# Performance work log

Measured on AMD Instinct MI355X. Metric: run time of the kernel, lower is better.

The kernel has to match this reference:

```python
import jax, jax.numpy as jnp
import numpy as np

N, IN_FEATS, H_FEATS, N_LAYERS, TOP_K, M = 8192, 512, 256, 2, 16, 65536


def setup_inputs() -> dict:
    key = jax.random.key(0)
    ks = jax.random.split(key, 16)
    s = 0.05
    return {
        "src": jax.random.randint(ks[0], (M,), 0, N, dtype=jnp.int32),
        "dst": jax.random.randint(ks[1], (M,), 0, N, dtype=jnp.int32),
        "labels": jax.random.uniform(ks[2], (M,), dtype=jnp.float32),
        "adj": jax.random.uniform(ks[3], (N, N), dtype=jnp.float32),
        "x": jax.random.normal(ks[4], (N, IN_FEATS), dtype=jnp.float32),
        # GNN1 layer weights
        "W1_0": jax.random.normal(ks[5], (IN_FEATS, H_FEATS), dtype=jnp.float32) * s,
        "W1_1": jax.random.normal(ks[6], (H_FEATS, H_FEATS), dtype=jnp.float32) * s,
        # GNN2 layer weights
        "W2_0": jax.random.normal(ks[7], (IN_FEATS, H_FEATS), dtype=jnp.float32) * s,
        "W2_1": jax.random.normal(ks[8], (H_FEATS, H_FEATS), dtype=jnp.float32) * s,
        # similarity-graph attention params
        "W": jax.random.normal(ks[9], (IN_FEATS, H_FEATS), dtype=jnp.float32) * s,
        "a1": jax.random.normal(ks[10], (H_FEATS, 1), dtype=jnp.float32) * s,
        "a2": jax.random.normal(ks[11], (H_FEATS, 1), dtype=jnp.float32) * s,
        # bilinear head: weight [1, in_feats, 2*h_feats], bias [1]
        "bil_w": jax.random.normal(ks[12], (1, IN_FEATS, 2 * H_FEATS), dtype=jnp.float32) * s,
        "bil_b": jnp.zeros((1,), dtype=jnp.float32),
    }


def _adj_norm(a):
    n = a.shape[0]
    a = a + jnp.eye(n, dtype=a.dtype)
    deg = a.sum(axis=0)[:, None]  # column sums, shape [n,1] (matches torch sum(dim=0).unsqueeze(1))
    return a / deg


def _gcn(a, x, weights):
    an = _adj_norm(a)
    z = x
    for Wl in weights:  # dropout=0.0 -> identity
        z = jax.nn.elu(an @ (z @ Wl))
    return z


def _sim_graph(x, W, a1, a2, top_k):
    n = x.shape[0]
    h = x @ W                      # [n, h]
    s1 = h @ a1                    # [n, 1]
    s2 = (h @ a2).reshape(1, n)    # [1, n]
    a = s1 + s2 - jnp.eye(n, dtype=x.dtype) * 1e15
    a = jax.nn.softmax(jax.nn.leaky_relu(a, 0.2), axis=1)
    kth = jax.lax.top_k(a, top_k)[0][:, -1:]  # k-th largest per row
    m = a >= kth
    m = m | m.T
    return m.astype(x.dtype)


def reference(src, dst, labels, adj, x, W1_0, W1_1, W2_0, W2_1, W, a1, a2, bil_w, bil_b):
    h = _gcn(adj, x, [W1_0, W1_1])
    sim_adj = _sim_graph(x, W, a1, a2, TOP_K)
    h_ = _gcn(sim_adj, x, [W2_0, W2_1])
    h_cat = jnp.concatenate([h, h_], axis=1)          # [n, 2h]
    src_h = x[src]                                    # [m, in_feats]
    dst_h = h_cat[dst]                                # [m, 2h]
    logits = jnp.einsum('mi,ij,mj->m', src_h, bil_w[0], dst_h) + bil_b[0]
    # BCEWithLogitsLoss (mean), numerically stable
    loss = jnp.mean(jnp.maximum(logits, 0.0) - logits * labels + jnp.log1p(jnp.exp(-jnp.abs(logits))))
    predict = logits >= 0
    return (loss, logits, predict)
```

## Files before the change

### kernel.cpp

```cpp
#include <hip/hip_runtime.h>
#include <math.h>

#define NN    8192
#define FIN   512
#define HF    256
#define ME    65536

typedef _Float16 f16x8 __attribute__((ext_vector_type(8)));
typedef __fp16 pk16x2 __attribute__((ext_vector_type(2)));
typedef float f32x4  __attribute__((ext_vector_type(4)));

__device__ inline void split_pk(float a0, float a1, unsigned& hi, unsigned& lo) {
    pk16x2 h = __builtin_amdgcn_cvt_pkrtz(a0, a1);
    float r0 = a0 - (float)h[0];
    float r1 = a1 - (float)h[1];
    pk16x2 l = __builtin_amdgcn_cvt_pkrtz(r0, r1);
    hi = __builtin_bit_cast(unsigned, h);
    lo = __builtin_bit_cast(unsigned, l);
}
__device__ inline unsigned pack_f16rn(float a0, float a1) {
    _Float16 h0 = (_Float16)a0, h1 = (_Float16)a1;
    unsigned u0 = (unsigned)__builtin_bit_cast(unsigned short, h0);
    unsigned u1 = (unsigned)__builtin_bit_cast(unsigned short, h1);
    return u0 | (u1 << 16);
}
__device__ inline unsigned short f16rn(float v) {
    return __builtin_bit_cast(unsigned short, (_Float16)v);
}
__device__ inline void split_f16(float v, short& hi, short& lo) {
    _Float16 h = (_Float16)v;
    _Float16 l = (_Float16)(v - (float)h);
    hi = __builtin_bit_cast(short, h);
    lo = __builtin_bit_cast(short, l);
}
__device__ inline float eluf(float v) { return v > 0.f ? v : expm1f(v); }

__device__ inline void gload16(const void* g, void* l) {
    __builtin_amdgcn_global_load_lds(
        (const __attribute__((address_space(1))) unsigned int*)g,
        (__attribute__((address_space(3))) unsigned int*)l, 16, 0, 0);
}

__global__ __launch_bounds__(256) void colsum_cv(const float* __restrict__ adj,
                                                 float* __restrict__ deg,
                                                 unsigned short* __restrict__ adjh) {
    int c = (blockIdx.x * 256 + threadIdx.x) * 4;
    int r0 = blockIdx.y * 64;
    float4 s = make_float4(0.f, 0.f, 0.f, 0.f);
    for (int r = r0; r < r0 + 64; ++r) {
        float4 v = *(const float4*)(adj + (size_t)r * NN + c);
        s.x += v.x; s.y += v.y; s.z += v.z; s.w += v.w;
        if (adjh) {
            ushort4 h;
            h.x = f16rn(v.x); h.y = f16rn(v.y); h.z = f16rn(v.z); h.w = f16rn(v.w);
            *(ushort4*)(adjh + (size_t)r * NN + c) = h;
        }
    }
    if (blockIdx.y == 0) { s.x += 1.f; s.y += 1.f; s.z += 1.f; s.w += 1.f; }
    atomicAdd(&deg[c + 0], s.x);
    atomicAdd(&deg[c + 1], s.y);
    atomicAdd(&deg[c + 2], s.z);
    atomicAdd(&deg[c + 3], s.w);
}

__global__ __launch_bounds__(256) void trans_w_split(const float* __restrict__ src,
                                                     short* __restrict__ dsth,
                                                     short* __restrict__ dstl,
                                                     int K, int lgN) {
    int idx = blockIdx.x * 256 + threadIdx.x;
    int N = 1 << lgN;
    int k = idx >> lgN, n = idx & (N - 1);
    short h, l;
    split_f16(src[idx], h, l);
    dsth[(size_t)n * K + k] = h;
    dstl[(size_t)n * K + k] = l;
}

template <int PASSES, int WBT>
__global__ __launch_bounds__(256, 2) void mfma_gemm(
    const float* __restrict__ A, const short* __restrict__ BtH,
    const short* __restrict__ BtL, float* __restrict__ C,
    short* __restrict__ CtH, short* __restrict__ CtL, int M, int K, int N)
{
    __shared__ __align__(16) char smem[49152];
    char* sAh = smem;
    char* sAl = smem + 8192;
    char* sBh = smem + 16384;
    char* sBl = smem + 32768;
    float* sT = (float*)smem;
    const int tid = threadIdx.x, lane = tid & 63, wid = tid >> 6;
    const int wm = wid >> 1, wn = wid & 1;
    const int m0 = blockIdx.x * 64, n0 = blockIdx.y * 128;
    const int lhi = lane >> 4, llo = lane & 15;

    f32x4 acc[2][4];
    #pragma unroll
    for (int mi = 0; mi < 2; ++mi)
        #pragma unroll
        for (int ni = 0; ni < 4; ++ni) acc[mi][ni] = (f32x4){0.f, 0.f, 0.f, 0.f};

    for (int kt = 0; kt < K; kt += 64) {
        float4 av[4];
        #pragma unroll
        for (int it = 0; it < 4; ++it) {
            int h = tid + 256 * it;
            int r = h >> 4, hs = h & 15, slot = hs >> 1, half = hs & 1;
            int gk = ((slot ^ (r & 7)) * 2 + half) * 4;
            av[it] = *(const float4*)(A + (size_t)(m0 + r) * K + kt + gk);
        }
        __syncthreads();
        #pragma unroll
        for (int it = 0; it < 4; ++it) {
            int u = tid + 256 * it;
            int c = u >> 3, s = u & 7;
            size_t off = (size_t)(n0 + c) * K + kt + (s ^ (c & 7)) * 8;
            gload16(BtH + off, sBh + u * 16);
            gload16(BtL + off, sBl + u * 16);
        }
        #pragma unroll
        for (int it = 0; it < 4; ++it) {
            int h = tid + 256 * it;
            if (PASSES == 3) {
                uint2 wh, wl;
                split_pk(av[it].x, av[it].y, wh.x, wl.x);
                split_pk(av[it].z, av[it].w, wh.y, wl.y);
                *(uint2*)(sAh + h * 8) = wh;
                *(uint2*)(sAl + h * 8) = wl;
            } else {
                uint2 wh;
                wh.x = pack_f16rn(av[it].x, av[it].y);
                wh.y = pack_f16rn(av[it].z, av[it].w);
                *(uint2*)(sAh + h * 8) = wh;
            }
        }
        __syncthreads();
        #pragma unroll
        for (int ks = 0; ks < 2; ++ks) {
            f16x8 afh[2], afl[2], bfh[4], bfl[4];
            #pragma unroll
            for (int mi = 0; mi < 2; ++mi) {
                int R = wm * 32 + mi * 16 + llo;
                int boff = R * 128 + (((ks * 4 + lhi) ^ (R & 7)) << 4);
                afh[mi] = *(const f16x8*)(sAh + boff);
                if (PASSES == 3) afl[mi] = *(const f16x8*)(sAl + boff);
            }
            #pragma unroll
            for (int ni = 0; ni < 4; ++ni) {
                int Cc = wn * 64 + ni * 16 + llo;
                int boff = Cc * 128 + (((ks * 4 + lhi) ^ (Cc & 7)) << 4);
                bfh[ni] = *(const f16x8*)(sBh + boff);
                bfl[ni] = *(const f16x8*)(sBl + boff);
            }
            #pragma unroll
            for (int mi = 0; mi < 2; ++mi)
                #pragma unroll
                for (int ni = 0; ni < 4; ++ni) {
                    acc[mi][ni] = __builtin_amdgcn_mfma_f32_16x16x32_f16(afh[mi], bfh[ni], acc[mi][ni], 0, 0, 0);
                    acc[mi][ni] = __builtin_amdgcn_mfma_f32_16x16x32_f16(afh[mi], bfl[ni], acc[mi][ni], 0, 0, 0);
                    if (PASSES == 3)
                        acc[mi][ni] = __builtin_amdgcn_mfma_f32_16x16x32_f16(afl[mi], bfh[ni], acc[mi][ni], 0, 0, 0);
                }
        }
    }

    if (WBT) {
        __syncthreads();
        #pragma unroll
        for (int mi = 0; mi < 2; ++mi)
            #pragma unroll
            for (int ni = 0; ni < 4; ++ni) {
                int lr = wm * 32 + mi * 16 + lhi * 4;
                int lc = wn * 64 + ni * 16 + llo;
                int R0 = m0 + lr;
                int Cc = n0 + lc;
                #pragma unroll
                for (int r = 0; r < 4; ++r) {
                    C[(size_t)(R0 + r) * N + Cc] = acc[mi][ni][r];
                    sT[(lr + r) * 136 + lc] = acc[mi][ni][r];
                }
            }
        __syncthreads();
        int c = tid >> 1, ih = (tid & 1) * 32;
        unsigned bh[16], bl[16];
        #pragma unroll
        for (int j = 0; j < 32; j += 2)
            split_pk(sT[(ih + j) * 136 + c], sT[(ih + j + 1) * 136 + c],
                     bh[j >> 1], bl[j >> 1]);
        int4* dh = (int4*)(CtH + (size_t)(n0 + c) * M + m0 + ih);
        int4* dl = (int4*)(CtL + (size_t)(n0 + c) * M + m0 + ih);
        #pragma unroll
        for (int q = 0; q < 4; ++q) { dh[q] = ((int4*)bh)[q]; dl[q] = ((int4*)bl)[q]; }
    } else {
        #pragma unroll
        for (int mi = 0; mi < 2; ++mi)
            #pragma unroll
            for (int ni = 0; ni < 4; ++ni) {
                int R0 = m0 + wm * 32 + mi * 16 + lhi * 4;
                int Cc = n0 + wn * 64 + ni * 16 + llo;
                #pragma unroll
                for (int r = 0; r < 4; ++r)
                    C[(size_t)(R0 + r) * N + Cc] = acc[mi][ni][r];
            }
    }
}

__global__ __launch_bounds__(256, 4) void adj_prop_g(const unsigned short* __restrict__ adjh,
                                                     const short* __restrict__ YtH,
                                                     const short* __restrict__ YtL,
                                                     float* part0, float* part1)
{
    __shared__ __align__(16) char smem[24576];
    const int tid = threadIdx.x, lane = tid & 63, wid = tid >> 6;
    const int wm = wid >> 1, wn = wid & 1;
    const int bid = blockIdx.x;
    const int g  = bid & 7;
    const int ky = g >> 2;
    const int gx = g & 3;
    const int s  = bid >> 3;
    const int bm = gx * 32 + (s >> 2), bn = s & 3;
    const int i0 = bm * 64, c0 = bn * 64;
    const int kbase = ky * (NN / 2);
    const int lhi = lane >> 4, llo = lane & 15;

    f32x4 acc[2][2];
    #pragma unroll
    for (int mi = 0; mi < 2; ++mi)
        #pragma unroll
        for (int ni = 0; ni < 2; ++ni) acc[mi][ni] = (f32x4){0.f, 0.f, 0.f, 0.f};

    for (int t = 0; t < 64; ++t) {
        const int KT = kbase + t * 64;
        __syncthreads();
        #pragma unroll
        for (int it = 0; it < 2; ++it) {
            int u = tid + 256 * it;
            int r = u >> 3, sq = u & 7;
            gload16(adjh + (size_t)(i0 + r) * NN + KT + ((sq ^ (r & 7)) * 8),
                    smem + u * 16);
        }
        #pragma unroll
        for (int it = 0; it < 2; ++it) {
            int u = tid + 256 * it;
            int c = u >> 3, sq = u & 7;
            size_t off = (size_t)(c0 + c) * NN + KT + (sq ^ (c & 7)) * 8;
            gload16(YtH + off, smem + 8192 + u * 16);
            gload16(YtL + off, smem + 16384 + u * 16);
        }
        __syncthreads();
        {
            const char* ah = smem;
            const char* bh = smem + 8192;
            const char* bl = smem + 16384;
            #pragma unroll
            for (int ks = 0; ks < 2; ++ks) {
                f16x8 af[2], bfh[2], bfl[2];
                #pragma unroll
                for (int mi = 0; mi < 2; ++mi) {
                    int R = wm * 32 + mi * 16 + llo;
                    int boff = R * 128 + (((ks * 4 + lhi) ^ (R & 7)) << 4);
                    af[mi] = *(const f16x8*)(ah + boff);
                }
                #pragma unroll
                for (int ni = 0; ni < 2; ++ni) {
                    int Cc = wn * 32 + ni * 16 + llo;
                    int boff = Cc * 128 + (((ks * 4 + lhi) ^ (Cc & 7)) << 4);
                    bfh[ni] = *(const f16x8*)(bh + boff);
                    bfl[ni] = *(const f16x8*)(bl + boff);
                }
                #pragma unroll
                for (int mi = 0; mi < 2; ++mi)
                    #pragma unroll
                    for (int ni = 0; ni < 2; ++ni) {
                        acc[mi][ni] = __builtin_amdgcn_mfma_f32_16x16x32_f16(af[mi], bfh[ni], acc[mi][ni], 0, 0, 0);
                        acc[mi][ni] = __builtin_amdgcn_mfma_f32_16x16x32_f16(af[mi], bfl[ni], acc[mi][ni], 0, 0, 0);
                    }
            }
        }
    }

    __syncthreads();
    float* sT = (float*)smem;
    #pragma unroll
    for (int mi = 0; mi < 2; ++mi)
        #pragma unroll
        for (int ni = 0; ni < 2; ++ni) {
            int lr = wm * 32 + mi * 16 + lhi * 4;
            int lc = wn * 32 + ni * 16 + llo;
            #pragma unroll
            for (int r = 0; r < 4; ++r)
                sT[(lr + r) * 68 + lc] = acc[mi][ni][r];
        }
    __syncthreads();
    float* po = ky == 0 ? part0 : part1;
    int row = tid >> 2, quad = tid & 3;
    float4* prow = (float4*)(po + (size_t)(i0 + row) * HF + c0 + quad * 16);
    #pragma unroll
    for (int q = 0; q < 4; ++q)
        prow[q] = *(const float4*)&sT[row * 68 + quad * 16 + q * 4];
}

__global__ __launch_bounds__(256, 4) void adj_prop_cv(const float* __restrict__ adj,
                                                      const short* __restrict__ YtH,
                                                      const short* __restrict__ YtL,
                                                      float* part0, float* part1)
{
    __shared__ __align__(16) char smem[24576];
    const int tid = threadIdx.x, lane = tid & 63, wid = tid >> 6;
    const int wm = wid >> 1, wn = wid & 1;
    const int bid = blockIdx.x;
    const int g  = bid & 7;
    const int ky = g >> 2;
    const int gx = g & 3;
    const int s  = bid >> 3;
    const int bm = gx * 32 + (s >> 2), bn = s & 3;
    const int i0 = bm * 64, c0 = bn * 64;
    const int kbase = ky * (NN / 2);
    const int lhi = lane >> 4, llo = lane & 15;

    f32x4 acc[2][2];
    #pragma unroll
    for (int mi = 0; mi < 2; ++mi)
        #pragma unroll
        for (int ni = 0; ni < 2; ++ni) acc[mi][ni] = (f32x4){0.f, 0.f, 0.f, 0.f};

    float4 avA[4], avB[4];

#define LOAD_ADJ(KT, AV)                                                        \
    {                                                                           \
        _Pragma("unroll")                                                       \
        for (int it = 0; it < 4; ++it) {                                        \
            int h = tid + 256 * it;                                             \
            int r = h >> 4, hs = h & 15, slot = hs >> 1, half = hs & 1;         \
            int gk = ((slot ^ (r & 7)) * 2 + half) * 4;                         \
            AV[it] = *(const float4*)(adj + (size_t)(i0 + r) * NN + (KT) + gk); \
        }                                                                       \
    }
#define GLOAD_B(KT)                                                             \
    {                                                                           \
        _Pragma("unroll")                                                       \
        for (int it = 0; it < 2; ++it) {                                        \
            int u = tid + 256 * it;                                             \
            int c = u >> 3, s2 = u & 7;                                         \
            size_t off = (size_t)(c0 + c) * NN + (KT) + (s2 ^ (c & 7)) * 8;     \
            gload16(YtH + off, smem + 8192 + u * 16);                           \
            gload16(YtL + off, smem + 16384 + u * 16);                          \
        }                                                                       \
    }
#define CONVERT_A(AV)                                                           \
    {                                                                           \
        _Pragma("unroll")                                                       \
        for (int it = 0; it < 4; ++it) {                                        \
            int h = tid + 256 * it;                                             \
            uint2 wh;                                                           \
            wh.x = pack_f16rn(AV[it].x, AV[it].y);                              \
            wh.y = pack_f16rn(AV[it].z, AV[it].w);                              \
            *(uint2*)(smem + h * 8) = wh;                                       \
        }                                                                       \
    }
#define DO_MFMA()                                                               \
    {                                                                           \
        const char* ah = smem;                                                  \
        const char* bh = smem + 8192;                                           \
        const char* bl = smem + 16384;                                          \
        _Pragma("unroll")                                                       \
        for (int ks = 0; ks < 2; ++ks) {                                        \
            f16x8 af[2], bfh[2], bfl[2];                                        \
            _Pragma("unroll")                                                   \
            for (int mi = 0; mi < 2; ++mi) {                                    \
                int R = wm * 32 + mi * 16 + llo;                                \
                int boff = R * 128 + (((ks * 4 + lhi) ^ (R & 7)) << 4);         \
                af[mi] = *(const f16x8*)(ah + boff);                            \
            }                                                                   \
            _Pragma("unroll")                                                   \
            for (int ni = 0; ni < 2; ++ni) {                                    \
                int Cc = wn * 32 + ni * 16 + llo;                               \
                int boff = Cc * 128 + (((ks * 4 + lhi) ^ (Cc & 7)) << 4);       \
                bfh[ni] = *(const f16x8*)(bh + boff);                           \
                bfl[ni] = *(const f16x8*)(bl + boff);                           \
            }                                                                   \
            _Pragma("unroll")                                                   \
            for (int mi = 0; mi < 2; ++mi)                                      \
                _Pragma("unroll")                                               \
                for (int ni = 0; ni < 2; ++ni) {                                \
                    acc[mi][ni] = __builtin_amdgcn_mfma_f32_16x16x32_f16(af[mi], bfh[ni], acc[mi][ni], 0, 0, 0); \
                    acc[mi][ni] = __builtin_amdgcn_mfma_f32_16x16x32_f16(af[mi], bfl[ni], acc[mi][ni], 0, 0, 0); \
                }                                                               \
        }                                                                       \
    }

    LOAD_ADJ(kbase, avA);
    LOAD_ADJ(kbase + 64, avB);
    for (int t = 0; t < 64; t += 2) {
        __syncthreads();
        GLOAD_B(kbase + t * 64);
        CONVERT_A(avA);
        __syncthreads();
        if (t + 2 < 64) LOAD_ADJ(kbase + (t + 2) * 64, avA);
        DO_MFMA();
        __syncthreads();
        GLOAD_B(kbase + (t + 1) * 64);
        CONVERT_A(avB);
        __syncthreads();
        if (t + 3 < 64) LOAD_ADJ(kbase + (t + 3) * 64, avB);
        DO_MFMA();
    }
#undef LOAD_ADJ
#undef GLOAD_B
#undef CONVERT_A
#undef DO_MFMA

    __syncthreads();
    float* sT = (float*)smem;
    #pragma unroll
    for (int mi = 0; mi < 2; ++mi)
        #pragma unroll
        for (int ni = 0; ni < 2; ++ni) {
            int lr = wm * 32 + mi * 16 + lhi * 4;
            int lc = wn * 32 + ni * 16 + llo;
            #pragma unroll
            for (int r = 0; r < 4; ++r)
                sT[(lr + r) * 68 + lc] = acc[mi][ni][r];
        }
    __syncthreads();
    float* po = ky == 0 ? part0 : part1;
    int row = tid >> 2, quad = tid & 3;
    float4* prow = (float4*)(po + (size_t)(i0 + row) * HF + c0 + quad * 16);
    #pragma unroll
    for (int q = 0; q < 4; ++q)
        prow[q] = *(const float4*)&sT[row * 68 + quad * 16 + q * 4];
}

__global__ __launch_bounds__(256) void adj_reduce(const float* part0,
                                                  const float* part1,
                                                  const float* __restrict__ Y,
                                                  const float* __restrict__ deg,
                                                  float* H) {
    int idx = blockIdx.x * 256 + threadIdx.x;
    int i = idx >> 6;
    float4 p0 = ((const float4*)part0)[idx];
    float4 p1 = ((const float4*)part1)[idx];
    float4 y  = ((const float4*)Y)[idx];
    float dinv = 1.f / deg[i];
    float4 v;
    v.x = eluf((p0.x + p1.x + y.x) * dinv);
    v.y = eluf((p0.y + p1.y + y.y) * dinv);
    v.z = eluf((p0.z + p1.z + y.z) * dinv);
    v.w = eluf((p0.w + p1.w + y.w) * dinv);
    ((float4*)H)[idx] = v;
}

__global__ __launch_bounds__(512) void wa2_kernel(const float* __restrict__ W,
                                                  const float* __restrict__ a2,
                                                  float* __restrict__ wa2) {
    int i = threadIdx.x;
    float s = 0.f;
    for (int j = 0; j < HF; ++j) s += W[(size_t)i * HF + j] * a2[j];
    wa2[i] = s;
}

__global__ __launch_bounds__(256) void s2_kernel(const float* __restrict__ x,
                                                 const float* __restrict__ wa2,
                                                 float* __restrict__ s2) {
    int lane = threadIdx.x & 63, wv = threadIdx.x >> 6;
    int row = blockIdx.x * 4 + wv;
    const float4* xr = (const float4*)(x + (size_t)row * FIN);
    const float4* w4 = (const float4*)wa2;
    float s = 0.f;
    #pragma unroll
    for (int t = 0; t < 2; ++t) {
        float4 a = xr[lane + 64 * t], b = w4[lane + 64 * t];
        s += a.x * b.x + a.y * b.y + a.z * b.z + a.w * b.w;
    }
    #pragma unroll
    for (int off = 32; off > 0; off >>= 1) s += __shfl_down(s, off);
    if (lane == 0) s2[row] = s;
}

__global__ __launch_bounds__(256) void top16_kernel(const float* __restrict__ s2,
                                                    int* __restrict__ Tflag) {
    __shared__ float sv[NN];
    __shared__ float rv[256];
    __shared__ int   ri[256];
    int tid = threadIdx.x;
    for (int i = tid; i < NN; i += 256) sv[i] = s2[i];
    __syncthreads();
    for (int it = 0; it < 16; ++it) {
        float best = -INFINITY; int bi = NN;
        for (int i = tid; i < NN; i += 256) {
            float v = sv[i];
            if (v > best) { best = v; bi = i; }
        }
        rv[tid] = best; ri[tid] = bi;
        __syncthreads();
        for (int off = 128; off > 0; off >>= 1) {
            if (tid < off) {
                float v2 = rv[tid + off]; int i2 = ri[tid + off];
                if (v2 > rv[tid] || (v2 == rv[tid] && i2 < ri[tid])) {
                    rv[tid] = v2; ri[tid] = i2;
                }
            }
            __syncthreads();
        }
        if (tid == 0) { int wi = ri[0]; Tflag[wi] = 1; sv[wi] = -INFINITY; }
        __syncthreads();
    }
}

__global__ __launch_bounds__(256) void colsum_T(const float* __restrict__ Y,
                                                const int* __restrict__ Tflag,
                                                float* __restrict__ total,
                                                float* __restrict__ sumT) {
    int k = threadIdx.x;
    int r0 = blockIdx.x * 128;
    float t = 0.f, tt = 0.f;
    for (int r = r0; r < r0 + 128; ++r) {
        float v = Y[(size_t)r * HF + k];
        t += v;
        if (Tflag[r]) tt += v;
    }
    atomicAdd(&total[k], t);
    atomicAdd(&sumT[k], tt);
}

__global__ __launch_bounds__(256) void gcn2_combine(float* __restrict__ Y,
                                                    const int* __restrict__ Tflag,
                                                    const float* __restrict__ sumT,
                                                    const float* __restrict__ total) {
    int idx = blockIdx.x * 256 + threadIdx.x;
    int i = idx >> 8, k = idx & 255;
    float v;
    if (Tflag[i]) v = total[k] / 8192.0f;
    else          v = (sumT[k] + Y[idx]) / 17.0f;
    Y[idx] = v > 0.f ? v : expm1f(v);
}

__global__ __launch_bounds__(256) void bilinear_kernel(
    const float* __restrict__ XB, const float* __restrict__ H,
    const float* __restrict__ Hs, const int* __restrict__ src,
    const int* __restrict__ dst, const float* __restrict__ labels,
    const float* __restrict__ bil_b,
    float* __restrict__ out_logits, float* __restrict__ out_pred,
    float* __restrict__ partials)
{
    __shared__ float wterm[4];
    int lane = threadIdx.x & 63;
    int wv = threadIdx.x >> 6;
    int e = blockIdx.x * 4 + wv;
    int s = src[e], d = dst[e];
    const float4* xb = (const float4*)(XB + (size_t)s * 512);
    const float4* h1 = (const float4*)(H + (size_t)d * HF);
    const float4* h2 = (const float4*)(Hs + (size_t)d * HF);
    float4 a = xb[lane], b = h1[lane];
    float sum = a.x * b.x + a.y * b.y + a.z * b.z + a.w * b.w;
    a = xb[64 + lane]; b = h2[lane];
    sum += a.x * b.x + a.y * b.y + a.z * b.z + a.w * b.w;
    #pragma unroll
    for (int off = 32; off > 0; off >>= 1) sum += __shfl_down(sum, off);
    if (lane == 0) {
        float l = sum + bil_b[0];
        out_logits[e] = l;
        out_pred[e] = (l >= 0.f) ? 1.f : 0.f;
        float lab = labels[e];
        wterm[wv] = fmaxf(l, 0.f) - l * lab + log1pf(expf(-fabsf(l)));
    }
    __syncthreads();
    if (threadIdx.x == 0)
        partials[blockIdx.x] = wterm[0] + wterm[1] + wterm[2] + wterm[3];
}

__global__ __launch_bounds__(256) void loss_finalize(const float* __restrict__ partials,
                                                     float* __restrict__ out) {
    __shared__ float s[256];
    int tid = threadIdx.x;
    float t = 0.f;
    for (int i = tid; i < ME / 4; i += 256) t += partials[i];
    s[tid] = t; __syncthreads();
    for (int off = 128; off > 0; off >>= 1) {
        if (tid < off) s[tid] += s[tid + off];
        __syncthreads();
    }
    if (tid == 0) out[0] = s[0] * (1.0f / (float)ME);
}

extern "C" void kernel_launch(void* const* d_in, const int* in_sizes, int n_in,
                              void* d_out, int out_size, void* d_ws, size_t ws_size,
                              hipStream_t stream) {
    const int*   src    = (const int*)d_in[0];
    const int*   dst    = (const int*)d_in[1];
    const float* labels = (const float*)d_in[2];
    const float* adj    = (const float*)d_in[3];
    const float* x      = (const float*)d_in[4];
    const float* W1_0   = (const float*)d_in[5];
    const float* W1_1   = (const float*)d_in[6];
    const float* W2_0   = (const float*)d_in[7];
    const float* W2_1   = (const float*)d_in[8];
    const float* W      = (const float*)d_in[9];
    const float* a2     = (const float*)d_in[11];
    const float* bilw   = (const float*)d_in[12];
    const float* bilb   = (const float*)d_in[13];

    float* w = (float*)d_ws;
    float* deg    = w + 0;
    float* s2v    = w + 8192;
    float* wa2v   = w + 16384;
    float* sumT   = w + 16896;
    float* total  = w + 17152;
    float* sum2T  = w + 17408;
    float* tot2   = w + 17664;
    float* lossp  = w + 17920;
    int*   Tflag  = (int*)(w + 34304);
    short* W10tH  = (short*)(w + 42496);
    short* W10tL  = (short*)(w + 108032);
    short* W11tH  = (short*)(w + 173568);
    short* W11tL  = (short*)(w + 206336);
    short* W20tH  = (short*)(w + 239104);
    short* W20tL  = (short*)(w + 304640);
    short* W21tH  = (short*)(w + 370176);
    short* W21tL  = (short*)(w + 402944);
    short* bilwtH = (short*)(w + 435712);
    short* bilwtL = (short*)(w + 566784);
    float* bufY   = w + 697856;
    short* YbtH   = (short*)(w + 2795008);
    short* YbtL   = (short*)(w + 3843584);
    float* bufH1  = w + 4892160;
    float* bufH   = w + 6989312;
    float* bufHs  = w + 9086464;
    unsigned short* adjh = (unsigned short*)(w + 11183616);
    float* XB     = bufY;
    const bool big = ws_size >= (size_t)44738048 * sizeof(float);

    float* out       = (float*)d_out;
    float* out_logit = out + 1;
    float* out_pred  = out + 1 + ME;

    hipMemsetAsync(deg, 0, NN * sizeof(float), stream);
    hipMemsetAsync(sumT, 0, 1024 * sizeof(float), stream);
    hipMemsetAsync(Tflag, 0, NN * sizeof(int), stream);

    trans_w_split<<<512, 256, 0, stream>>>(W1_0, W10tH, W10tL, 512, 8);
    trans_w_split<<<256, 256, 0, stream>>>(W1_1, W11tH, W11tL, 256, 8);
    trans_w_split<<<512, 256, 0, stream>>>(W2_0, W20tH, W20tL, 512, 8);
    trans_w_split<<<256, 256, 0, stream>>>(W2_1, W21tH, W21tL, 256, 8);
    trans_w_split<<<1024, 256, 0, stream>>>(bilw, bilwtH, bilwtL, 512, 9);

    colsum_cv<<<dim3(8, 128), 256, 0, stream>>>(adj, deg, big ? adjh : nullptr);

    mfma_gemm<2, 1><<<dim3(128, 2), 256, 0, stream>>>(x, W10tH, W10tL, bufY, YbtH, YbtL, NN, FIN, HF);
    if (big) adj_prop_g<<<1024, 256, 0, stream>>>(adjh, YbtH, YbtL, bufH, bufHs);
    else     adj_prop_cv<<<1024, 256, 0, stream>>>(adj, YbtH, YbtL, bufH, bufHs);
    adj_reduce<<<2048, 256, 0, stream>>>(bufH, bufHs, bufY, deg, bufH1);
    mfma_gemm<2, 1><<<dim3(128, 2), 256, 0, stream>>>(bufH1, W11tH, W11tL, bufY, YbtH, YbtL, NN, HF, HF);
    if (big) adj_prop_g<<<1024, 256, 0, stream>>>(adjh, YbtH, YbtL, bufH, bufHs);
    else     adj_prop_cv<<<1024, 256, 0, stream>>>(adj, YbtH, YbtL, bufH, bufHs);
    adj_reduce<<<2048, 256, 0, stream>>>(bufH, bufHs, bufY, deg, bufH);

    wa2_kernel<<<1, 512, 0, stream>>>(W, a2, wa2v);
    s2_kernel<<<NN / 4, 256, 0, stream>>>(x, wa2v, s2v);
    top16_kernel<<<1, 256, 0, stream>>>(s2v, Tflag);

    mfma_gemm<3, 0><<<dim3(128, 2), 256, 0, stream>>>(x, W20tH, W20tL, bufY,
                                                      (short*)nullptr, (short*)nullptr, NN, 512, 256);
    colsum_T<<<64, 256, 0, stream>>>(bufY, Tflag, total, sumT);
    gcn2_combine<<<NN, 256, 0, stream>>>(bufY, Tflag, sumT, total);
    mfma_gemm<3, 0><<<dim3(128, 2), 256, 0, stream>>>(bufY, W21tH, W21tL, bufHs,
                                                      (short*)nullptr, (short*)nullptr, NN, 256, 256);
    colsum_T<<<64, 256, 0, stream>>>(bufHs, Tflag, tot2, sum2T);
    gcn2_combine<<<NN, 256, 0, stream>>>(bufHs, Tflag, sum2T, tot2);

    mfma_gemm<3, 0><<<dim3(128, 4), 256, 0, stream>>>(x, bilwtH, bilwtL, XB,
                                                      (short*)nullptr, (short*)nullptr, NN, 512, 512);
    bilinear_kernel<<<ME / 4, 256, 0, stream>>>(XB, bufH, bufHs, src, dst, labels, bilb,
                                                out_logit, out_pred, lossp);
    loss_finalize<<<1, 256, 0, stream>>>(lossp, out);
}
```

Before: 541.6 us.

## Double-buffer LDS tiles in adj_prop_g and unroll colsum row loop

The adjacency-propagation GEMM kernel gets two 24 KB LDS buffers. The direct-to-LDS loads for the next K tile are issued before the MFMA work on the current tile, with one barrier per iteration, so load latency can overlap compute instead of serialising. This doubles shared memory per block, and the occupancy hint drops from 4 to 3 blocks per CU, which may cost latency hiding and cause a tail wave. Separately, the column-sum/fp16-convert kernel processes two rows per iteration with split accumulators to expose more memory-level parallelism.

```diff
diff --git a/kernel.cpp b/kernel.cpp
--- a/kernel.cpp
+++ b/kernel.cpp
@@ -46,16 +46,22 @@
                                                  unsigned short* __restrict__ adjh) {
     int c = (blockIdx.x * 256 + threadIdx.x) * 4;
     int r0 = blockIdx.y * 64;
-    float4 s = make_float4(0.f, 0.f, 0.f, 0.f);
-    for (int r = r0; r < r0 + 64; ++r) {
-        float4 v = *(const float4*)(adj + (size_t)r * NN + c);
-        s.x += v.x; s.y += v.y; s.z += v.z; s.w += v.w;
+    float4 s0 = make_float4(0.f, 0.f, 0.f, 0.f);
+    float4 s1 = make_float4(0.f, 0.f, 0.f, 0.f);
+    for (int r = r0; r < r0 + 64; r += 2) {
+        float4 v0 = *(const float4*)(adj + (size_t)r * NN + c);
+        float4 v1 = *(const float4*)(adj + (size_t)(r + 1) * NN + c);
+        s0.x += v0.x; s0.y += v0.y; s0.z += v0.z; s0.w += v0.w;
+        s1.x += v1.x; s1.y += v1.y; s1.z += v1.z; s1.w += v1.w;
         if (adjh) {
-            ushort4 h;
-            h.x = f16rn(v.x); h.y = f16rn(v.y); h.z = f16rn(v.z); h.w = f16rn(v.w);
-            *(ushort4*)(adjh + (size_t)r * NN + c) = h;
-        }
-    }
+            ushort4 h0, h1;
+            h0.x = f16rn(v0.x); h0.y = f16rn(v0.y); h0.z = f16rn(v0.z); h0.w = f16rn(v0.w);
+            h1.x = f16rn(v1.x); h1.y = f16rn(v1.y); h1.z = f16rn(v1.z); h1.w = f16rn(v1.w);
+            *(ushort4*)(adjh + (size_t)r * NN + c) = h0;
+            *(ushort4*)(adjh + (size_t)(r + 1) * NN + c) = h1;
+        }
+    }
+    float4 s = make_float4(s0.x + s1.x, s0.y + s1.y, s0.z + s1.z, s0.w + s1.w);
     if (blockIdx.y == 0) { s.x += 1.f; s.y += 1.f; s.z += 1.f; s.w += 1.f; }
     atomicAdd(&deg[c + 0], s.x);
     atomicAdd(&deg[c + 1], s.y);
@@ -204,12 +210,12 @@
     }
 }
 
-__global__ __launch_bounds__(256, 4) void adj_prop_g(const unsigned short* __restrict__ adjh,
+__global__ __launch_bounds__(256, 3) void adj_prop_g(const unsigned short* __restrict__ adjh,
                                                      const short* __restrict__ YtH,
                                                      const short* __restrict__ YtL,
                                                      float* part0, float* part1)
 {
-    __shared__ __align__(16) char smem[24576];
+    __shared__ __align__(16) char smem[49152];
     const int tid = threadIdx.x, lane = tid & 63, wid = tid >> 6;
     const int wm = wid >> 1, wn = wid & 1;
     const int bid = blockIdx.x;
@@ -228,29 +234,36 @@
         #pragma unroll
         for (int ni = 0; ni < 2; ++ni) acc[mi][ni] = (f32x4){0.f, 0.f, 0.f, 0.f};
 
+#define ISSUE_DMA(T, B)                                                         \
+    {                                                                           \
+        const int KT = kbase + (T) * 64;                                        \
+        char* base = smem + (B) * 24576;                                        \
+        _Pragma("unroll")                                                       \
+        for (int it = 0; it < 2; ++it) {                                        \
+            int u = tid + 256 * it;                                             \
+            int r = u >> 3, sq = u & 7;                                         \
+            gload16(adjh + (size_t)(i0 + r) * NN + KT + ((sq ^ (r & 7)) * 8),   \
+                    base + u * 16);                                             \
+        }                                                                       \
+        _Pragma("unroll")                                                       \
+        for (int it = 0; it < 2; ++it) {                                        \
+            int u = tid + 256 * it;                                             \
+            int c = u >> 3, sq = u & 7;                                         \
+            size_t off = (size_t)(c0 + c) * NN + KT + (sq ^ (c & 7)) * 8;       \
+            gload16(YtH + off, base + 8192 + u * 16);                           \
+            gload16(YtL + off, base + 16384 + u * 16);                          \
+        }                                                                       \
+    }
+
+    ISSUE_DMA(0, 0);
+    __syncthreads();
     for (int t = 0; t < 64; ++t) {
-        const int KT = kbase + t * 64;
-        __syncthreads();
-        #pragma unroll
-        for (int it = 0; it < 2; ++it) {
-            int u = tid + 256 * it;
-            int r = u >> 3, sq = u & 7;
-            gload16(adjh + (size_t)(i0 + r) * NN + KT + ((sq ^ (r & 7)) * 8),
-                    smem + u * 16);
-        }
-        #pragma unroll
-        for (int it = 0; it < 2; ++it) {
-            int u = tid + 256 * it;
-            int c = u >> 3, sq = u & 7;
-            size_t off = (size_t)(c0 + c) * NN + KT + (sq ^ (c & 7)) * 8;
-            gload16(YtH + off, smem + 8192 + u * 16);
-            gload16(YtL + off, smem + 16384 + u * 16);
-        }
-        __syncthreads();
+        const int cur = t & 1;
+        if (t + 1 < 64) ISSUE_DMA(t + 1, cur ^ 1);
         {
-            const char* ah = smem;
-            const char* bh = smem + 8192;
-            const char* bl = smem + 16384;
+            const char* ah = smem + cur * 24576;
+            const char* bh = ah + 8192;
+            const char* bl = ah + 16384;
             #pragma unroll
             for (int ks = 0; ks < 2; ++ks) {
                 f16x8 af[2], bfh[2], bfl[2];
@@ -276,9 +289,10 @@
                     }
             }
         }
-    }
-
-    __syncthreads();
+        __syncthreads();
+    }
+#undef ISSUE_DMA
+
     float* sT = (float*)smem;
     #pragma unroll
     for (int mi = 0; mi < 2; ++mi)
```

Result: slower. 562.4 us (+3.8%).
